# Performance work log

Hardware: AMD Instinct MI355X
Metric: run time of the kernel (lower is better)

The kernel has to match this reference:

```python
import jax, jax.numpy as jnp
import numpy as np

D = 1024
H = 16
HD = D // H
DS = 64
B, L = 2, 2048


def setup_inputs() -> dict:
    key = jax.random.key(0)
    ks = jax.random.split(key, 12)
    s = 0.02
    return {
        "x": jax.random.normal(ks[0], (B, L, D), jnp.float32),
        "subject_embed": jax.random.normal(ks[1], (B, DS), jnp.float32),
        "key_padding_mask": jnp.zeros((B, L), jnp.bool_),
        "Wq": jax.random.normal(ks[2], (D, D), jnp.float32) * s,
        "Wk": jax.random.normal(ks[3], (D, D), jnp.float32) * s,
        "Wv": jax.random.normal(ks[4], (D, D), jnp.float32) * s,
        "Wo": jax.random.normal(ks[5], (D, D), jnp.float32) * s,
        "bo": jnp.zeros((D,), jnp.float32),
        "Wsq": jax.random.normal(ks[6], (DS, D), jnp.float32) * s,
        "bsq": jnp.zeros((D,), jnp.float32),
        "Wsk": jax.random.normal(ks[7], (DS, D), jnp.float32) * s,
        "bsk": jnp.zeros((D,), jnp.float32),
    }


def reference(x, subject_embed, key_padding_mask, Wq, Wk, Wv, Wo, bo, Wsq, bsq, Wsk, bsk):
    scale = 1.0 / jnp.sqrt(jnp.asarray(HD, x.dtype))
    q = x @ Wq + (subject_embed @ Wsq + bsq)[:, None, :]   # [B,L,D]
    k = x @ Wk + (subject_embed @ Wsk + bsk)[:, None, :]
    v = x @ Wv
    # split heads: [B,H,L,hd]
    q = q.reshape(B, L, H, HD).transpose(0, 2, 1, 3)
    k = k.reshape(B, L, H, HD).transpose(0, 2, 1, 3)
    v = v.reshape(B, L, H, HD).transpose(0, 2, 1, 3)
    attn = jnp.einsum('bhqd,bhkd->bhqk', q, k) * scale      # [B,H,L,L]
    attn = jnp.where(key_padding_mask[:, None, None, :], -jnp.inf, attn)
    attn = jax.nn.softmax(attn, axis=-1)
    out = jnp.einsum('bhqk,bhkd->bhqd', attn, v)
    out = out.transpose(0, 2, 1, 3).reshape(B, L, D)
    return out @ Wo + bo
```

## Files before the change

### kernel.cpp

```cpp
#include <hip/hip_runtime.h>
#include <hip/hip_bf16.h>
#include <math.h>

#define DEV __device__ __forceinline__

typedef short bf16x8 __attribute__((ext_vector_type(8)));
typedef short bf16x4 __attribute__((ext_vector_type(4)));
typedef float f32x4 __attribute__((ext_vector_type(4)));

static constexpr int D  = 1024;
static constexpr int H  = 16;
static constexpr int HD = 64;
static constexpr int DS = 64;
static constexpr int B  = 2;
static constexpr int L  = 2048;
static constexpr int M  = B * L;

static constexpr float QSCALE = 0.18033688011112042f;

DEV unsigned short f2bf(float f) {
  union { float f; unsigned u; } x; x.f = f;
  unsigned r = (x.u + 0x7FFFu + ((x.u >> 16) & 1u)) >> 16;
  return (unsigned short)r;
}

DEV unsigned pack2bf(float a, float b) {
  return (unsigned)f2bf(a) | ((unsigned)f2bf(b) << 16);
}

DEV unsigned pack2bf_trunc(float a, float b) {
  union { float f; unsigned u; } ua{a}, ub{b};
  return __builtin_amdgcn_perm(ub.u, ua.u, 0x07060302u);
}

DEV void gload_lds16(const void* g, void* l) {
  __builtin_amdgcn_global_load_lds(
      (const __attribute__((address_space(1))) unsigned int*)g,
      (__attribute__((address_space(3))) unsigned int*)l, 16, 0, 0);
}

__global__ __launch_bounds__(256) void prep_kernel(
    const float* __restrict__ Wq, const float* __restrict__ Wk,
    const float* __restrict__ Wv, const float* __restrict__ Wo,
    const float* __restrict__ x, const float* __restrict__ subj,
    const float* __restrict__ Wsq, const float* __restrict__ bsq,
    const float* __restrict__ Wsk, const float* __restrict__ bsk,
    unsigned short* __restrict__ WT4, unsigned short* __restrict__ xb,
    float* __restrict__ sq, float* __restrict__ sk) {
  __shared__ float tile[64][65];
  const int blk = blockIdx.x, t = threadIdx.x;
  if (blk < 1024) {
    const int z = blk >> 8, idx = blk & 255;
    const float* W = z == 0 ? Wq : z == 1 ? Wk : z == 2 ? Wv : Wo;
    unsigned short* dst = WT4 + (size_t)z * D * D;
    const int n0 = (idx & 15) * 64, k0 = (idx >> 4) * 64;
    const int c4 = (t & 15) * 4;
    const int r16 = t >> 4;
#pragma unroll
    for (int rr = 0; rr < 4; ++rr) {
      int row = r16 + rr * 16;
      float4 v = *(const float4*)&W[(size_t)(k0 + row) * D + n0 + c4];
      tile[row][c4 + 0] = v.x;
      tile[row][c4 + 1] = v.y;
      tile[row][c4 + 2] = v.z;
      tile[row][c4 + 3] = v.w;
    }
    __syncthreads();
#pragma unroll
    for (int rr = 0; rr < 4; ++rr) {
      int nrow = r16 + rr * 16;
      ushort4 u;
      u.x = f2bf(tile[c4 + 0][nrow]);
      u.y = f2bf(tile[c4 + 1][nrow]);
      u.z = f2bf(tile[c4 + 2][nrow]);
      u.w = f2bf(tile[c4 + 3][nrow]);
      *(ushort4*)&dst[(size_t)(n0 + nrow) * D + k0 + c4] = u;
    }
  } else if (blk < 3072) {
    size_t g = (size_t)(blk - 1024) * 256 + t;
    const float4* xf = (const float4*)x;
    float4 a = xf[2 * g], b = xf[2 * g + 1];
    union { unsigned short s[8]; uint4 v; } o;
    o.s[0] = f2bf(a.x); o.s[1] = f2bf(a.y); o.s[2] = f2bf(a.z); o.s[3] = f2bf(a.w);
    o.s[4] = f2bf(b.x); o.s[5] = f2bf(b.y); o.s[6] = f2bf(b.z); o.s[7] = f2bf(b.w);
    ((uint4*)xb)[g] = o.v;
  } else {
    int g = (blk - 3072) * 256 + t;
    int ty = g >> 11, b = (g >> 10) & 1, n = g & 1023;
    const float* W = ty ? Wsk : Wsq;
    const float* bias = ty ? bsk : bsq;
    float s = bias[n];
#pragma unroll 8
    for (int d = 0; d < DS; ++d) s += subj[b * DS + d] * W[d * D + n];
    (ty ? sk : sq)[b * D + n] = s;
  }
}

__global__ __launch_bounds__(256) void proj_kernel(
    const unsigned short* __restrict__ xb, const unsigned short* __restrict__ WT3,
    const float* __restrict__ sq, const float* __restrict__ sk,
    unsigned short* __restrict__ qk, unsigned short* __restrict__ vT) {
  __shared__ __align__(16) unsigned short smem[40960];
  const int lin = blockIdx.x + 8 * blockIdx.y;
  const int x8 = lin & 7, c = lin >> 3;
  const int mt = (x8 & 3) * 8 + (c >> 3);
  const int nt = (x8 >> 2) * 8 + (c & 7);
  const int m0 = mt * 128, n0 = nt * 64;
  const int t = threadIdx.x, l = t & 63, w = t >> 6;
  const int lm = l & 15, lq = l >> 4;
  const int srow8 = t >> 3;
  const int fsw = ((t & 7) ^ ((t >> 3) & 7)) * 8;
  const int swm = lm & 7;

  auto stage = [&](int kt, int bsel) {
    const int kb = kt * 64;
    unsigned short* As = smem + bsel * 20480;
    unsigned short* Bs = As + 8192;
#pragma unroll
    for (int cc = 0; cc < 4; ++cc)
      gload_lds16(&xb[(size_t)(m0 + 32 * cc + srow8) * D + kb + fsw],
                  &As[(32 * cc + 8 * w) * 64]);
#pragma unroll
    for (int z = 0; z < 3; ++z)
#pragma unroll
      for (int cc = 0; cc < 2; ++cc)
        gload_lds16(&WT3[(size_t)z * D * D + (size_t)(n0 + 32 * cc + srow8) * D + kb + fsw],
                    &Bs[z * 4096 + (32 * cc + 8 * w) * 64]);
  };

  f32x4 acc[3][2][4] = {};
  stage(0, 0);
  __syncthreads();
  for (int kt = 0; kt < D / 64; ++kt) {
    const int cur = kt & 1;
    if (kt + 1 < D / 64) stage(kt + 1, cur ^ 1);
    const unsigned short* As = smem + cur * 20480;
    const unsigned short* Bs = As + 8192;
#pragma unroll
    for (int kk = 0; kk < 2; ++kk) {
      bf16x8 af[2];
#pragma unroll
      for (int i = 0; i < 2; ++i)
        af[i] = *(const bf16x8*)&As[(32 * w + 16 * i + lm) * 64 + ((kk * 4 + lq) ^ swm) * 8];
#pragma unroll
      for (int z = 0; z < 3; ++z)
#pragma unroll
        for (int j = 0; j < 4; ++j) {
          bf16x8 bfj = *(const bf16x8*)&Bs[z * 4096 + (16 * j + lm) * 64 + ((kk * 4 + lq) ^ swm) * 8];
#pragma unroll
          for (int i = 0; i < 2; ++i)
            acc[z][i][j] = __builtin_amdgcn_mfma_f32_16x16x32_bf16(af[i], bfj, acc[z][i][j], 0, 0, 0);
        }
    }
    __syncthreads();
  }

  const int bb = m0 >> 11;
  const int l0 = m0 & (L - 1);
  const int h0 = nt;

#pragma unroll
  for (int z = 0; z < 2; ++z) {
    const float* bias = z == 0 ? sq : sk;
    const float post = z == 0 ? QSCALE : 1.0f;
    unsigned short* dst = qk + (size_t)z * M * D;
#pragma unroll
    for (int i = 0; i < 2; ++i)
#pragma unroll
      for (int j = 0; j < 4; ++j)
#pragma unroll
        for (int r = 0; r < 4; ++r) {
          int rr = 32 * w + 16 * i + 4 * lq + r;
          int cc = 16 * j + lm;
          float v = (acc[z][i][j][r] + bias[bb * D + n0 + cc]) * post;
          smem[rr * 72 + cc] = f2bf(v);
        }
    __syncthreads();
    const int row = t >> 1, half = t & 1;
    size_t dbase = ((size_t)(bb * H + h0) * L + l0 + row) * HD + half * 32;
#pragma unroll
    for (int cq = 0; cq < 4; ++cq) {
      uint4 u = *(const uint4*)&smem[row * 72 + half * 32 + cq * 8];
      *(uint4*)&dst[dbase + cq * 8] = u;
    }
    __syncthreads();
  }

#pragma unroll
  for (int i = 0; i < 2; ++i)
#pragma unroll
    for (int j = 0; j < 4; ++j) {
      int cr = 16 * j + lm;
      int rr = 32 * w + 16 * i + 4 * lq;
      uint2 u;
      u.x = pack2bf(acc[2][i][j][0], acc[2][i][j][1]);
      u.y = pack2bf(acc[2][i][j][2], acc[2][i][j][3]);
      *(uint2*)&smem[cr * 136 + rr] = u;
    }
  __syncthreads();
  {
    const int cr = t >> 2, quarter = t & 3;
    size_t dbase = ((size_t)(bb * H + h0) * HD + cr) * L + l0 + quarter * 32;
#pragma unroll
    for (int cq = 0; cq < 4; ++cq) {
      uint4 u = *(const uint4*)&smem[cr * 136 + quarter * 32 + cq * 8];
      *(uint4*)&vT[dbase + cq * 8] = u;
    }
  }
}

__global__ __launch_bounds__(512, 4) void attn_kernel(
    const unsigned short* __restrict__ q_hm, const unsigned short* __restrict__ k_hm,
    const unsigned short* __restrict__ vT, const unsigned char* __restrict__ mask,
    unsigned short* __restrict__ ctx) {
  __shared__ __align__(16) unsigned short smem[40960];
  unsigned short* Qs  = smem;
  unsigned short* Ksb = smem + 8192;
  unsigned short* Vtb = smem + 24576;
  const int bx = blockIdx.x;
  const int rest = bx >> 3;
  const int bhid = (bx & 7) + 8 * (rest >> 4);
  const int q0 = (rest & 15) * 128;
  const int h = bhid & 15, b = bhid >> 4;
  const size_t bh = (size_t)(b * H + h);
  const unsigned short* qp = q_hm + bh * L * HD;
  const unsigned short* kp = k_hm + bh * L * HD;
  const unsigned short* vp = vT + bh * HD * L;
  const int t = threadIdx.x, l = t & 63, w = t >> 6;
  const int wq = w & 3, wj = w >> 2;
  const int lm = l & 15, lq = l >> 4;
  const int fsw = ((t & 7) ^ ((t >> 3) & 7)) * 8;
  const int swm = lm & 7;
  const int srow = t >> 3;
  const int vs = t & 15, vr = t >> 4;
  const int vcsrc = ((vs & 8) | ((vs & 7) ^ (vr & 7))) * 8;
  const int krow0 = 8 * (lm >> 2) + 4 * ((lm >> 2) & 1) + (lm & 3);
  const int ks0 = krow0 & 7;
  const int krow1 = krow0 ^ 4;
  const int ks1 = ks0 ^ 4;
  const bf16x8 vones = {(short)0x3F80, (short)0x3F80, (short)0x3F80, (short)0x3F80,
                        (short)0x3F80, (short)0x3F80, (short)0x3F80, (short)0x3F80};

#pragma unroll
  for (int c = 0; c < 2; ++c) {
    gload_lds16(&qp[(size_t)(q0 + 64 * c + srow) * HD + fsw], &Qs[(64 * c + 8 * w) * 64]);
    gload_lds16(&kp[(size_t)(64 * c + srow) * HD + fsw], &Ksb[(64 * c + 8 * w) * 64]);
    gload_lds16(&vp[(size_t)(32 * c + vr) * L + vcsrc], &Vtb[(32 * c + 4 * w) * 128]);
  }
  __syncthreads();
  bf16x8 qf[2][2];
#pragma unroll
  for (int i = 0; i < 2; ++i)
#pragma unroll
    for (int kk = 0; kk < 2; ++kk)
      qf[i][kk] = *(const bf16x8*)&Qs[(wq * 32 + 16 * i + lm) * 64 + ((kk * 4 + lq) ^ swm) * 8];

  f32x4 ot[2][4] = {};
  f32x4 ot1[2] = {};

  for (int kt = 0; kt < L / 128; ++kt) {
    const int cur = kt & 1;
    const unsigned short* Kc = Ksb + cur * 8192;
    const unsigned short* Vc = Vtb + cur * 8192;
    unsigned char mby = mask[b * L + kt * 128 + 64 * wj + l];
    if (kt + 1 < L / 128) {
      const int nk0 = (kt + 1) * 128;
      unsigned short* Kd = Ksb + (cur ^ 1) * 8192;
      unsigned short* Vd = Vtb + (cur ^ 1) * 8192;
#pragma unroll
      for (int c = 0; c < 2; ++c) {
        gload_lds16(&kp[(size_t)(nk0 + 64 * c + srow) * HD + fsw], &Kd[(64 * c + 8 * w) * 64]);
        gload_lds16(&vp[(size_t)(32 * c + vr) * L + nk0 + vcsrc], &Vd[(32 * c + 4 * w) * 128]);
      }
    }
    unsigned long long mb = __ballot(mby != 0);

#pragma unroll
    for (int g = 0; g < 2; ++g) {
      const int gg = 2 * wj + g;
      const unsigned short* Kg = Kc + 32 * gg * 64;
      bf16x8 ka0 = *(const bf16x8*)&Kg[krow0 * 64 + ((0 + lq) ^ ks0) * 8];
      bf16x8 ka1 = *(const bf16x8*)&Kg[krow0 * 64 + ((4 + lq) ^ ks0) * 8];
      bf16x8 kb0 = *(const bf16x8*)&Kg[krow1 * 64 + ((0 + lq) ^ ks1) * 8];
      bf16x8 kb1 = *(const bf16x8*)&Kg[krow1 * 64 + ((4 + lq) ^ ks1) * 8];
      f32x4 stA[2], stB[2];
      __builtin_amdgcn_s_setprio(1);
#pragma unroll
      for (int i = 0; i < 2; ++i) {
        f32x4 a = {};
        a = __builtin_amdgcn_mfma_f32_16x16x32_bf16(ka0, qf[i][0], a, 0, 0, 0);
        a = __builtin_amdgcn_mfma_f32_16x16x32_bf16(ka1, qf[i][1], a, 0, 0, 0);
        stA[i] = a;
        f32x4 bq = {};
        bq = __builtin_amdgcn_mfma_f32_16x16x32_bf16(kb0, qf[i][0], bq, 0, 0, 0);
        bq = __builtin_amdgcn_mfma_f32_16x16x32_bf16(kb1, qf[i][1], bq, 0, 0, 0);
        stB[i] = bq;
      }
      __builtin_amdgcn_s_setprio(0);
      if (mb) {
        const int shA = 32 * g + 8 * lq + 4 * (lq & 1);
        unsigned bitsA = (unsigned)(mb >> shA);
        unsigned bitsB = (unsigned)(mb >> (shA ^ 4));
#pragma unroll
        for (int i = 0; i < 2; ++i)
#pragma unroll
          for (int r = 0; r < 4; ++r) {
            if ((bitsA >> r) & 1u) stA[i][r] = -1e30f;
            if ((bitsB >> r) & 1u) stB[i][r] = -1e30f;
          }
      }
      union { uint4 q; bf16x8 v; } pa[2];
      const bool sw = (lq & 1) != 0;
#pragma unroll
      for (int i = 0; i < 2; ++i) {
        float eA[4], eB[4];
#pragma unroll
        for (int r = 0; r < 4; ++r) {
          eA[r] = __builtin_amdgcn_exp2f(stA[i][r]);
          eB[r] = __builtin_amdgcn_exp2f(stB[i][r]);
        }
        unsigned a01 = pack2bf_trunc(eA[0], eA[1]);
        unsigned a23 = pack2bf_trunc(eA[2], eA[3]);
        unsigned b01 = pack2bf_trunc(eB[0], eB[1]);
        unsigned b23 = pack2bf_trunc(eB[2], eB[3]);
        pa[i].q.x = sw ? b01 : a01;
        pa[i].q.y = sw ? b23 : a23;
        pa[i].q.z = sw ? a01 : b01;
        pa[i].q.w = sw ? a23 : b23;
      }
      const int kc = 4 * gg + lq;
      const int slot = (kc & 8) | ((kc & 7) ^ swm);
      __builtin_amdgcn_s_setprio(1);
#pragma unroll
      for (int jf = 0; jf < 4; ++jf) {
        bf16x8 vb = *(const bf16x8*)&Vc[(16 * jf + lm) * 128 + slot * 8];
#pragma unroll
        for (int i = 0; i < 2; ++i)
          ot[i][jf] = __builtin_amdgcn_mfma_f32_16x16x32_bf16(pa[i].v, vb, ot[i][jf], 0, 0, 0);
      }
#pragma unroll
      for (int i = 0; i < 2; ++i)
        ot1[i] = __builtin_amdgcn_mfma_f32_16x16x32_bf16(pa[i].v, vones, ot1[i], 0, 0, 0);
      __builtin_amdgcn_s_setprio(0);
    }
    __syncthreads();
  }

  float* Obuf = (float*)smem;
  unsigned short* Es = smem + 20480;
  float* Sred = (float*)(smem + 35840);

  if (lm == 0) {
#pragma unroll
    for (int i = 0; i < 2; ++i)
#pragma unroll
      for (int r = 0; r < 4; ++r)
        Sred[w * 32 + 16 * i + 4 * lq + r] = ot1[i][r];
  }
  if (wj) {
#pragma unroll
    for (int i = 0; i < 2; ++i)
#pragma unroll
      for (int jf = 0; jf < 4; ++jf)
        *(f32x4*)&Obuf[(16 * jf + lm) * 132 + wq * 32 + 16 * i + 4 * lq] = ot[i][jf];
  }
  __syncthreads();
  if (!wj) {
    float rlq[2][4];
#pragma unroll
    for (int i = 0; i < 2; ++i)
#pragma unroll
      for (int r = 0; r < 4; ++r)
        rlq[i][r] = 1.0f / (ot1[i][r] + Sred[(w + 4) * 32 + 16 * i + 4 * lq + r]);
#pragma unroll
    for (int i = 0; i < 2; ++i)
#pragma unroll
      for (int jf = 0; jf < 4; ++jf) {
        f32x4 po = *(const f32x4*)&Obuf[(16 * jf + lm) * 132 + wq * 32 + 16 * i + 4 * lq];
        ot[i][jf] += po;
      }
#pragma unroll
    for (int i = 0; i < 2; ++i)
#pragma unroll
      for (int jf = 0; jf < 4; ++jf)
#pragma unroll
        for (int r = 0; r < 4; ++r)
          Es[(wq * 32 + 16 * i + 4 * lq + r) * 72 + 16 * jf + lm] =
              f2bf(ot[i][jf][r] * rlq[i][r]);
    int row = l >> 1, half = l & 1;
    size_t obase = ((size_t)(b * L + q0 + wq * 32 + row)) * D + h * HD + half * 32;
#pragma unroll
    for (int c = 0; c < 4; ++c) {
      uint4 u = *(const uint4*)&Es[(wq * 32 + row) * 72 + half * 32 + c * 8];
      *(uint4*)&ctx[obase + c * 8] = u;
    }
  }
}

__global__ __launch_bounds__(256) void outgemm_kernel(
    const unsigned short* __restrict__ ctx, const unsigned short* __restrict__ WoT,
    const float* __restrict__ bo, float* __restrict__ out) {
  __shared__ __align__(16) unsigned short smem[24576];
  const int lin = blockIdx.x + 8 * blockIdx.y;
  const int nlin = (lin & 7) * 64 + (lin >> 3);
  const int m0 = (nlin >> 3) * 64, n0 = (nlin & 7) * 128;
  const int t = threadIdx.x, l = t & 63, w = t >> 6;
  const int wm = w >> 1, wn = w & 1;
  const int lm = l & 15, lq = l >> 4;
  const int srow8 = t >> 3;
  const int fsw = ((t & 7) ^ ((t >> 3) & 7)) * 8;
  const int swm = lm & 7;

  auto stage = [&](int kt, int bsel) {
    const int kb = kt * 64;
    unsigned short* As = smem + bsel * 12288;
    unsigned short* Bs = As + 4096;
#pragma unroll
    for (int c = 0; c < 2; ++c)
      gload_lds16(&ctx[(size_t)(m0 + 32 * c + srow8) * D + kb + fsw],
                  &As[(32 * c + 8 * w) * 64]);
#pragma unroll
    for (int c = 0; c < 4; ++c)
      gload_lds16(&WoT[(size_t)(n0 + 32 * c + srow8) * D + kb + fsw],
                  &Bs[(32 * c + 8 * w) * 64]);
  };

  f32x4 acc[2][4] = {};
  stage(0, 0);
  __syncthreads();
  for (int kt = 0; kt < D / 64; ++kt) {
    const int cur = kt & 1;
    if (kt + 1 < D / 64) stage(kt + 1, cur ^ 1);
    const unsigned short* As = smem + cur * 12288;
    const unsigned short* Bs = As + 4096;
#pragma unroll
    for (int kk = 0; kk < 2; ++kk) {
      bf16x8 af[2], bf[4];
#pragma unroll
      for (int i = 0; i < 2; ++i)
        af[i] = *(const bf16x8*)&As[(32 * wm + 16 * i + lm) * 64 + ((kk * 4 + lq) ^ swm) * 8];
#pragma unroll
      for (int j = 0; j < 4; ++j)
        bf[j] = *(const bf16x8*)&Bs[(64 * wn + 16 * j + lm) * 64 + ((kk * 4 + lq) ^ swm) * 8];
#pragma unroll
      for (int i = 0; i < 2; ++i)
#pragma unroll
        for (int j = 0; j < 4; ++j)
          acc[i][j] = __builtin_amdgcn_mfma_f32_16x16x32_bf16(af[i], bf[j], acc[i][j], 0, 0, 0);
    }
    __syncthreads();
  }
#pragma unroll
  for (int i = 0; i < 2; ++i)
#pragma unroll
    for (int j = 0; j < 4; ++j)
#pragma unroll
      for (int r = 0; r < 4; ++r) {
        int grow = m0 + 32 * wm + 16 * i + lq * 4 + r;
        int gcol = n0 + 64 * wn + 16 * j + lm;
        out[(size_t)grow * D + gcol] = acc[i][j][r] + bo[gcol];
      }
}

extern "C" void kernel_launch(void* const* d_in, const int* in_sizes, int n_in,
                              void* d_out, int out_size, void* d_ws, size_t ws_size,
                              hipStream_t stream) {
  const float* x    = (const float*)d_in[0];
  const float* subj = (const float*)d_in[1];
  const unsigned char* mask = (const unsigned char*)d_in[2];
  const float* Wq = (const float*)d_in[3];
  const float* Wk = (const float*)d_in[4];
  const float* Wv = (const float*)d_in[5];
  const float* Wo = (const float*)d_in[6];
  const float* bo = (const float*)d_in[7];
  const float* Wsq = (const float*)d_in[8];
  const float* bsq = (const float*)d_in[9];
  const float* Wsk = (const float*)d_in[10];
  const float* bsk = (const float*)d_in[11];
  float* out = (float*)d_out;
  char* ws = (char*)d_ws;

  unsigned short* xb  = (unsigned short*)(ws);
  unsigned short* WT4 = (unsigned short*)(ws + (8ull  << 20));
  unsigned short* qk  = (unsigned short*)(ws + (16ull << 20));
  unsigned short* ctx = (unsigned short*)(ws + (32ull << 20));
  unsigned short* vT  = (unsigned short*)(ws + (40ull << 20));
  float* sq = (float*)(ws + (48ull << 20));
  float* sk = sq + B * D;

  hipLaunchKernelGGL(prep_kernel, dim3(3088), dim3(256), 0, stream,
                     Wq, Wk, Wv, Wo, x, subj, Wsq, bsq, Wsk, bsk, WT4, xb, sq, sk);
  hipLaunchKernelGGL(proj_kernel, dim3(8, 64, 1), dim3(256), 0, stream,
                     xb, WT4, sq, sk, qk, vT);
  hipLaunchKernelGGL(attn_kernel, dim3(512), dim3(512), 0, stream,
                     qk, qk + (size_t)M * D, vT, mask, ctx);
  hipLaunchKernelGGL(outgemm_kernel, dim3(8, 64, 1), dim3(256), 0, stream, ctx,
                     WT4 + 3ull * D * D, bo, out);
}
```

Baseline: 188.3 us.

## Shrink attention tiles to 64 queries per 4-wave block, dropping split-key reduction

The attention kernel now uses 256-thread blocks that each handle 64 queries, with one 16-row query slice per wave. Keys are processed in 64-key double-buffered tiles, and every wave covers all keys. This removes the cross-wave partial-sum reduction through shared memory and halves LDS per block, doubling grid size for finer scheduling. In exchange, K/V tiles are reused across fewer queries, so global and LDS traffic per FLOP rises and there are twice as many barriers per key.

```diff
diff --git a/kernel.cpp b/kernel.cpp
--- a/kernel.cpp
+++ b/kernel.cpp
@@ -209,31 +209,28 @@
   }
 }
 
-__global__ __launch_bounds__(512, 4) void attn_kernel(
+__global__ __launch_bounds__(256) void attn_kernel(
     const unsigned short* __restrict__ q_hm, const unsigned short* __restrict__ k_hm,
     const unsigned short* __restrict__ vT, const unsigned char* __restrict__ mask,
     unsigned short* __restrict__ ctx) {
-  __shared__ __align__(16) unsigned short smem[40960];
+  __shared__ __align__(16) unsigned short smem[20480];
   unsigned short* Qs  = smem;
-  unsigned short* Ksb = smem + 8192;
-  unsigned short* Vtb = smem + 24576;
+  unsigned short* Ksb = smem + 4096;
+  unsigned short* Vtb = smem + 12288;
   const int bx = blockIdx.x;
   const int rest = bx >> 3;
-  const int bhid = (bx & 7) + 8 * (rest >> 4);
-  const int q0 = (rest & 15) * 128;
+  const int bhid = (bx & 7) + 8 * (rest >> 5);
+  const int q0 = (rest & 31) * 64;
   const int h = bhid & 15, b = bhid >> 4;
   const size_t bh = (size_t)(b * H + h);
   const unsigned short* qp = q_hm + bh * L * HD;
   const unsigned short* kp = k_hm + bh * L * HD;
   const unsigned short* vp = vT + bh * HD * L;
   const int t = threadIdx.x, l = t & 63, w = t >> 6;
-  const int wq = w & 3, wj = w >> 2;
   const int lm = l & 15, lq = l >> 4;
   const int fsw = ((t & 7) ^ ((t >> 3) & 7)) * 8;
   const int swm = lm & 7;
-  const int srow = t >> 3;
-  const int vs = t & 15, vr = t >> 4;
-  const int vcsrc = ((vs & 8) | ((vs & 7) ^ (vr & 7))) * 8;
+  const int srow8 = t >> 3;
   const int krow0 = 8 * (lm >> 2) + 4 * ((lm >> 2) & 1) + (lm & 3);
   const int ks0 = krow0 & 7;
   const int krow1 = krow0 ^ 4;
@@ -243,155 +240,106 @@
 
 #pragma unroll
   for (int c = 0; c < 2; ++c) {
-    gload_lds16(&qp[(size_t)(q0 + 64 * c + srow) * HD + fsw], &Qs[(64 * c + 8 * w) * 64]);
-    gload_lds16(&kp[(size_t)(64 * c + srow) * HD + fsw], &Ksb[(64 * c + 8 * w) * 64]);
-    gload_lds16(&vp[(size_t)(32 * c + vr) * L + vcsrc], &Vtb[(32 * c + 4 * w) * 128]);
+    gload_lds16(&qp[(size_t)(q0 + 32 * c + srow8) * HD + fsw], &Qs[(32 * c + 8 * w) * 64]);
+    gload_lds16(&kp[(size_t)(32 * c + srow8) * HD + fsw], &Ksb[(32 * c + 8 * w) * 64]);
+    gload_lds16(&vp[(size_t)(32 * c + srow8) * L + fsw], &Vtb[(32 * c + 8 * w) * 64]);
   }
   __syncthreads();
-  bf16x8 qf[2][2];
-#pragma unroll
-  for (int i = 0; i < 2; ++i)
-#pragma unroll
-    for (int kk = 0; kk < 2; ++kk)
-      qf[i][kk] = *(const bf16x8*)&Qs[(wq * 32 + 16 * i + lm) * 64 + ((kk * 4 + lq) ^ swm) * 8];
-
-  f32x4 ot[2][4] = {};
-  f32x4 ot1[2] = {};
-
-  for (int kt = 0; kt < L / 128; ++kt) {
+  bf16x8 qf[2];
+#pragma unroll
+  for (int kk = 0; kk < 2; ++kk)
+    qf[kk] = *(const bf16x8*)&Qs[(16 * w + lm) * 64 + ((kk * 4 + lq) ^ swm) * 8];
+
+  f32x4 ot[4] = {};
+  f32x4 ot1 = {};
+
+  for (int kt = 0; kt < L / 64; ++kt) {
     const int cur = kt & 1;
-    const unsigned short* Kc = Ksb + cur * 8192;
-    const unsigned short* Vc = Vtb + cur * 8192;
-    unsigned char mby = mask[b * L + kt * 128 + 64 * wj + l];
-    if (kt + 1 < L / 128) {
-      const int nk0 = (kt + 1) * 128;
-      unsigned short* Kd = Ksb + (cur ^ 1) * 8192;
-      unsigned short* Vd = Vtb + (cur ^ 1) * 8192;
+    const unsigned short* Kc = Ksb + cur * 4096;
+    const unsigned short* Vc = Vtb + cur * 4096;
+    unsigned char mby = mask[b * L + kt * 64 + l];
+    if (kt + 1 < L / 64) {
+      const int nk0 = (kt + 1) * 64;
+      unsigned short* Kd = Ksb + (cur ^ 1) * 4096;
+      unsigned short* Vd = Vtb + (cur ^ 1) * 4096;
 #pragma unroll
       for (int c = 0; c < 2; ++c) {
-        gload_lds16(&kp[(size_t)(nk0 + 64 * c + srow) * HD + fsw], &Kd[(64 * c + 8 * w) * 64]);
-        gload_lds16(&vp[(size_t)(32 * c + vr) * L + nk0 + vcsrc], &Vd[(32 * c + 4 * w) * 128]);
+        gload_lds16(&kp[(size_t)(nk0 + 32 * c + srow8) * HD + fsw], &Kd[(32 * c + 8 * w) * 64]);
+        gload_lds16(&vp[(size_t)(32 * c + srow8) * L + nk0 + fsw], &Vd[(32 * c + 8 * w) * 64]);
       }
     }
     unsigned long long mb = __ballot(mby != 0);
 
 #pragma unroll
     for (int g = 0; g < 2; ++g) {
-      const int gg = 2 * wj + g;
-      const unsigned short* Kg = Kc + 32 * gg * 64;
+      const unsigned short* Kg = Kc + 2048 * g;
       bf16x8 ka0 = *(const bf16x8*)&Kg[krow0 * 64 + ((0 + lq) ^ ks0) * 8];
       bf16x8 ka1 = *(const bf16x8*)&Kg[krow0 * 64 + ((4 + lq) ^ ks0) * 8];
       bf16x8 kb0 = *(const bf16x8*)&Kg[krow1 * 64 + ((0 + lq) ^ ks1) * 8];
       bf16x8 kb1 = *(const bf16x8*)&Kg[krow1 * 64 + ((4 + lq) ^ ks1) * 8];
-      f32x4 stA[2], stB[2];
+      f32x4 stA = {}, stB = {};
       __builtin_amdgcn_s_setprio(1);
-#pragma unroll
-      for (int i = 0; i < 2; ++i) {
-        f32x4 a = {};
-        a = __builtin_amdgcn_mfma_f32_16x16x32_bf16(ka0, qf[i][0], a, 0, 0, 0);
-        a = __builtin_amdgcn_mfma_f32_16x16x32_bf16(ka1, qf[i][1], a, 0, 0, 0);
-        stA[i] = a;
-        f32x4 bq = {};
-        bq = __builtin_amdgcn_mfma_f32_16x16x32_bf16(kb0, qf[i][0], bq, 0, 0, 0);
-        bq = __builtin_amdgcn_mfma_f32_16x16x32_bf16(kb1, qf[i][1], bq, 0, 0, 0);
-        stB[i] = bq;
-      }
+      stA = __builtin_amdgcn_mfma_f32_16x16x32_bf16(ka0, qf[0], stA, 0, 0, 0);
+      stA = __builtin_amdgcn_mfma_f32_16x16x32_bf16(ka1, qf[1], stA, 0, 0, 0);
+      stB = __builtin_amdgcn_mfma_f32_16x16x32_bf16(kb0, qf[0], stB, 0, 0, 0);
+      stB = __builtin_amdgcn_mfma_f32_16x16x32_bf16(kb1, qf[1], stB, 0, 0, 0);
       __builtin_amdgcn_s_setprio(0);
       if (mb) {
         const int shA = 32 * g + 8 * lq + 4 * (lq & 1);
         unsigned bitsA = (unsigned)(mb >> shA);
         unsigned bitsB = (unsigned)(mb >> (shA ^ 4));
 #pragma unroll
-        for (int i = 0; i < 2; ++i)
-#pragma unroll
-          for (int r = 0; r < 4; ++r) {
-            if ((bitsA >> r) & 1u) stA[i][r] = -1e30f;
-            if ((bitsB >> r) & 1u) stB[i][r] = -1e30f;
-          }
+        for (int r = 0; r < 4; ++r) {
+          if ((bitsA >> r) & 1u) stA[r] = -1e30f;
+          if ((bitsB >> r) & 1u) stB[r] = -1e30f;
+        }
       }
-      union { uint4 q; bf16x8 v; } pa[2];
+      union { uint4 q; bf16x8 v; } pa;
       const bool sw = (lq & 1) != 0;
-#pragma unroll
-      for (int i = 0; i < 2; ++i) {
-        float eA[4], eB[4];
-#pragma unroll
-        for (int r = 0; r < 4; ++r) {
-          eA[r] = __builtin_amdgcn_exp2f(stA[i][r]);
-          eB[r] = __builtin_amdgcn_exp2f(stB[i][r]);
-        }
-        unsigned a01 = pack2bf_trunc(eA[0], eA[1]);
-        unsigned a23 = pack2bf_trunc(eA[2], eA[3]);
-        unsigned b01 = pack2bf_trunc(eB[0], eB[1]);
-        unsigned b23 = pack2bf_trunc(eB[2], eB[3]);
-        pa[i].q.x = sw ? b01 : a01;
-        pa[i].q.y = sw ? b23 : a23;
-        pa[i].q.z = sw ? a01 : b01;
-        pa[i].q.w = sw ? a23 : b23;
+      float eA[4], eB[4];
+#pragma unroll
+      for (int r = 0; r < 4; ++r) {
+        eA[r] = __builtin_amdgcn_exp2f(stA[r]);
+        eB[r] = __builtin_amdgcn_exp2f(stB[r]);
       }
-      const int kc = 4 * gg + lq;
-      const int slot = (kc & 8) | ((kc & 7) ^ swm);
+      unsigned a01 = pack2bf_trunc(eA[0], eA[1]);
+      unsigned a23 = pack2bf_trunc(eA[2], eA[3]);
+      unsigned b01 = pack2bf_trunc(eB[0], eB[1]);
+      unsigned b23 = pack2bf_trunc(eB[2], eB[3]);
+      pa.q.x = sw ? b01 : a01;
+      pa.q.y = sw ? b23 : a23;
+      pa.q.z = sw ? a01 : b01;
+      pa.q.w = sw ? a23 : b23;
+      const int kc = 4 * g + lq;
+      const int slot = kc ^ swm;
       __builtin_amdgcn_s_setprio(1);
 #pragma unroll
       for (int jf = 0; jf < 4; ++jf) {
-        bf16x8 vb = *(const bf16x8*)&Vc[(16 * jf + lm) * 128 + slot * 8];
-#pragma unroll
-        for (int i = 0; i < 2; ++i)
-          ot[i][jf] = __builtin_amdgcn_mfma_f32_16x16x32_bf16(pa[i].v, vb, ot[i][jf], 0, 0, 0);
+        bf16x8 vb = *(const bf16x8*)&Vc[(16 * jf + lm) * 64 + slot * 8];
+        ot[jf] = __builtin_amdgcn_mfma_f32_16x16x32_bf16(pa.v, vb, ot[jf], 0, 0, 0);
       }
-#pragma unroll
-      for (int i = 0; i < 2; ++i)
-        ot1[i] = __builtin_amdgcn_mfma_f32_16x16x32_bf16(pa[i].v, vones, ot1[i], 0, 0, 0);
+      ot1 = __builtin_amdgcn_mfma_f32_16x16x32_bf16(pa.v, vones, ot1, 0, 0, 0);
       __builtin_amdgcn_s_setprio(0);
     }
     __syncthreads();
   }
 
-  float* Obuf = (float*)smem;
-  unsigned short* Es = smem + 20480;
-  float* Sred = (float*)(smem + 35840);
-
-  if (lm == 0) {
-#pragma unroll
-    for (int i = 0; i < 2; ++i)
-#pragma unroll
-      for (int r = 0; r < 4; ++r)
-        Sred[w * 32 + 16 * i + 4 * lq + r] = ot1[i][r];
-  }
-  if (wj) {
-#pragma unroll
-    for (int i = 0; i < 2; ++i)
-#pragma unroll
-      for (int jf = 0; jf < 4; ++jf)
-        *(f32x4*)&Obuf[(16 * jf + lm) * 132 + wq * 32 + 16 * i + 4 * lq] = ot[i][jf];
-  }
+  float rlq[4];
+#pragma unroll
+  for (int r = 0; r < 4; ++r) rlq[r] = 1.0f / ot1[r];
+  unsigned short* Es = smem;
+#pragma unroll
+  for (int jf = 0; jf < 4; ++jf)
+#pragma unroll
+    for (int r = 0; r < 4; ++r)
+      Es[(16 * w + 4 * lq + r) * 72 + 16 * jf + lm] = f2bf(ot[jf][r] * rlq[r]);
   __syncthreads();
-  if (!wj) {
-    float rlq[2][4];
-#pragma unroll
-    for (int i = 0; i < 2; ++i)
-#pragma unroll
-      for (int r = 0; r < 4; ++r)
-        rlq[i][r] = 1.0f / (ot1[i][r] + Sred[(w + 4) * 32 + 16 * i + 4 * lq + r]);
-#pragma unroll
-    for (int i = 0; i < 2; ++i)
-#pragma unroll
-      for (int jf = 0; jf < 4; ++jf) {
-        f32x4 po = *(const f32x4*)&Obuf[(16 * jf + lm) * 132 + wq * 32 + 16 * i + 4 * lq];
-        ot[i][jf] += po;
-      }
-#pragma unroll
-    for (int i = 0; i < 2; ++i)
-#pragma unroll
-      for (int jf = 0; jf < 4; ++jf)
-#pragma unroll
-        for (int r = 0; r < 4; ++r)
-          Es[(wq * 32 + 16 * i + 4 * lq + r) * 72 + 16 * jf + lm] =
-              f2bf(ot[i][jf][r] * rlq[i][r]);
-    int row = l >> 1, half = l & 1;
-    size_t obase = ((size_t)(b * L + q0 + wq * 32 + row)) * D + h * HD + half * 32;
-#pragma unroll
-    for (int c = 0; c < 4; ++c) {
-      uint4 u = *(const uint4*)&Es[(wq * 32 + row) * 72 + half * 32 + c * 8];
+  {
+    const int row = t >> 2, q4 = t & 3;
+    size_t obase = ((size_t)(b * L + q0 + row)) * D + h * HD + q4 * 16;
+#pragma unroll
+    for (int c = 0; c < 2; ++c) {
+      uint4 u = *(const uint4*)&Es[row * 72 + q4 * 16 + c * 8];
       *(uint4*)&ctx[obase + c * 8] = u;
     }
   }
@@ -492,7 +440,7 @@
                      Wq, Wk, Wv, Wo, x, subj, Wsq, bsq, Wsk, bsk, WT4, xb, sq, sk);
   hipLaunchKernelGGL(proj_kernel, dim3(8, 64, 1), dim3(256), 0, stream,
                      xb, WT4, sq, sk, qk, vT);
-  hipLaunchKernelGGL(attn_kernel, dim3(512), dim3(512), 0, stream,
+  hipLaunchKernelGGL(attn_kernel, dim3(1024), dim3(256), 0, stream,
                      qk, qk + (size_t)M * D, vT, mask, ctx);
   hipLaunchKernelGGL(outgemm_kernel, dim3(8, 64, 1), dim3(256), 0, stream, ctx,
                      WT4 + 3ull * D * D, bo, out);
```

After: 199.7 us. +6.1%, slower.
